# Kernel tuning notes

Hardware: AMD Instinct MI355X
Metric: run time of the kernel (lower is better)

## Reference

```python
import jax, jax.numpy as jnp
import numpy as np

C_IN, LAT, OUT, EMB = 3, 64, 512, 5
B, H = 128, 128
KS = [4, 4, 3, 4, 2]                       # per-layer dynamic kernel sizes
CHANS = [C_IN, LAT, LAT * 2, LAT * 4, LAT * 8]  # in-channels of each dyn conv
MIX = [(C_IN, LAT), (LAT, LAT * 2), (LAT * 2, LAT * 4), (LAT * 4, LAT * 8), (LAT * 8, OUT)]


def setup_inputs() -> dict:
    key = jax.random.key(0)
    ks = jax.random.split(key, 40)
    nrm = lambda k, shape, s=0.02: jax.random.normal(k, shape, jnp.float32) * s
    inp = {}
    inp["input"] = jax.random.normal(ks[0], (B, C_IN, H, H), jnp.float32)
    inp["label"] = jax.random.randint(ks[1], (B,), 0, 10)
    inp["emb"] = nrm(ks[2], (10, EMB), 1.0)  # label embedding table
    i = 3
    for j, (c, k) in enumerate(zip(CHANS, KS), 1):  # label -> dyn kernel linears
        inp[f"l{j}_w"] = nrm(ks[i], (EMB, c * k * k), 0.1)
        inp[f"l{j}_b"] = jnp.zeros((c * k * k,), jnp.float32)
        i += 1
    for j, (ci, co) in enumerate(MIX, 1):  # channel-mixer linears
        inp[f"cm{j}_w"] = nrm(ks[i], (ci, co))
        inp[f"cm{j}_b"] = jnp.zeros((co,), jnp.float32)
        i += 1
    for j, c in enumerate([LAT, LAT * 2, LAT * 4, LAT * 8], 1):  # BN affine params
        inp[f"bn{j}_g"] = jnp.ones((c,), jnp.float32)
        inp[f"bn{j}_b"] = jnp.zeros((c,), jnp.float32)
    return inp


def dw_conv(x, k, stride, pad):
    """Per-sample, per-channel (depthwise) 2d cross-correlation.
    x: (B,C,H,W), k: (B,C,h,w) -> (B,C,H',W')."""
    def one(xi, ki):
        return jax.lax.conv_general_dilated(
            xi[None], ki[:, None], (stride, stride),
            [(pad, pad), (pad, pad)],
            dimension_numbers=("NCHW", "OIHW", "NCHW"),
            feature_group_count=xi.shape[0])[0]
    return jax.vmap(one)(x, k)


def reference(input, label, emb,
              l1_w, l1_b, l2_w, l2_b, l3_w, l3_b, l4_w, l4_b, l5_w, l5_b,
              cm1_w, cm1_b, cm2_w, cm2_b, cm3_w, cm3_b, cm4_w, cm4_b, cm5_w, cm5_b,
              bn1_g, bn1_b, bn2_g, bn2_b, bn3_g, bn3_b, bn4_g, bn4_b):
    e = emb[label]  # (B, EMB)
    dk = lambda w, b, c, k: jnp.tanh(e @ w + b).reshape(-1, c, k, k)
    k1 = dk(l1_w, l1_b, C_IN, 4)
    k2 = dk(l2_w, l2_b, LAT, 4)
    k3 = dk(l3_w, l3_b, LAT * 2, 3)
    k4 = dk(l4_w, l4_b, LAT * 4, 4)
    k5 = dk(l5_w, l5_b, LAT * 8, 2)

    mix = lambda z, w, b: jnp.einsum("bchw,cd->bdhw", z, w) + b[None, :, None, None]
    lrelu = lambda z: jax.nn.leaky_relu(z, 0.2)

    def bn(z, g, b):  # training-mode BN (batch statistics, biased var, eps=1e-5)
        m = z.mean((0, 2, 3), keepdims=True)
        v = z.var((0, 2, 3), keepdims=True)
        return (z - m) * jax.lax.rsqrt(v + 1e-5) * g[None, :, None, None] + b[None, :, None, None]

    z = bn(lrelu(mix(dw_conv(input, k1, 2, 1), cm1_w, cm1_b)), bn1_g, bn1_b)
    z = bn(lrelu(mix(dw_conv(z, k2, 2, 1), cm2_w, cm2_b)), bn2_g, bn2_b)
    z = bn(lrelu(mix(dw_conv(z, k3, 2, 1), cm3_w, cm3_b)), bn3_g, bn3_b)
    z = bn(lrelu(mix(dw_conv(z, k4, 2, 1), cm4_w, cm4_b)), bn4_g, bn4_b)
    z = jax.nn.sigmoid(mix(dw_conv(z, k5, 1, 0), cm5_w, cm5_b))  # (B, OUT, 7, 7)
    return (z, label)
```

## Files before the change

### kernel.cpp

```cpp
#include <hip/hip_runtime.h>
#include <hip/hip_bf16.h>

typedef __hip_bfloat16 bf16;
using short8  = __attribute__((ext_vector_type(8))) short;
using floatx4 = __attribute__((ext_vector_type(4))) float;

__device__ __forceinline__ float b2f(unsigned short u) {
    union { unsigned int i; float f; } v; v.i = ((unsigned int)u) << 16; return v.f;
}
__device__ __forceinline__ unsigned short f2b(float f) {
    bf16 h = __float2bfloat16(f);
    return *(unsigned short*)&h;
}

#define NREP 16

__global__ __launch_bounds__(256) void prep_kernel(
    const int* __restrict__ label, const float* __restrict__ emb,
    const float* __restrict__ l1w, const float* __restrict__ l1b,
    const float* __restrict__ l2w, const float* __restrict__ l2b,
    const float* __restrict__ l3w, const float* __restrict__ l3b,
    const float* __restrict__ l4w, const float* __restrict__ l4b,
    const float* __restrict__ l5w, const float* __restrict__ l5b,
    float* __restrict__ dynk, float* __restrict__ stats,
    float* __restrict__ labelOut)
{
    const int tid = threadIdx.x;
    if (blockIdx.x == gridDim.x - 1) {
        for (int i = tid; i < 30720; i += 256) stats[i] = 0.0f;
        if (tid < 128) labelOut[tid] = (float)label[tid];
        return;
    }
    int idx = blockIdx.x * 256 + tid;
    if (idx >= 1071104) return;
    const float* w; const float* bb; int loc, ckk, ksk, base;
    if (idx < 6144)        { w = l1w; bb = l1b; loc = idx;          ckk = 48;   ksk = 0;  base = 0;      }
    else if (idx < 137216) { w = l2w; bb = l2b; loc = idx - 6144;   ckk = 1024; ksk = 16; base = 6144;   }
    else if (idx < 284672) { w = l3w; bb = l3b; loc = idx - 137216; ckk = 1152; ksk = 9;  base = 137216; }
    else if (idx < 808960) { w = l4w; bb = l4b; loc = idx - 284672; ckk = 4096; ksk = 16; base = 284672; }
    else                   { w = l5w; bb = l5b; loc = idx - 808960; ckk = 2048; ksk = 4;  base = 808960; }
    int b   = loc / ckk;
    int col = loc - b * ckk;
    int lab = label[b];
    float acc = bb[col];
    #pragma unroll
    for (int m = 0; m < 5; ++m)
        acc = fmaf(emb[lab * 5 + m], w[m * ckk + col], acc);
    float val = tanhf(acc);
    if (ksk == 0) {
        dynk[idx] = val;
    } else {
        int c  = col / ksk;
        int t  = col - c * ksk;
        int Cl = ckk / ksk;
        dynk[base + b * ckk + t * Cl + c] = val;
    }
}

__global__ void bn_prep(const float* __restrict__ st,
                        const float* __restrict__ gam, const float* __restrict__ bet,
                        float* __restrict__ aff, int C, float NINV)
{
    int c = threadIdx.x;
    if (c >= C) return;
    float s = 0.f, q = 0.f;
    #pragma unroll
    for (int r = 0; r < NREP; ++r) {
        s += st[r * 2 * C + c];
        q += st[r * 2 * C + C + c];
    }
    float m   = s * NINV;
    float var = fmaf(q, NINV, -m * m);
    float sc  = gam[c] * rsqrtf(var + 1e-5f);
    aff[c]     = sc;
    aff[C + c] = fmaf(-m, sc, bet[c]);
}

__global__ __launch_bounds__(256) void wt_kernel(
    const float* __restrict__ w2, const float* __restrict__ w3,
    const float* __restrict__ w4, const float* __restrict__ w5,
    bf16* __restrict__ wt2, bf16* __restrict__ wt3,
    bf16* __restrict__ wt4, bf16* __restrict__ wt5)
{
    __shared__ float T[32][33];
    const int tid = threadIdx.x;
    int t = blockIdx.x;
    const float* W; bf16* WT; int K, N, tl;
    if (t < 8)        { W = w2; WT = wt2; K = 64;  N = 128; tl = t; }
    else if (t < 40)  { W = w3; WT = wt3; K = 128; N = 256; tl = t - 8; }
    else if (t < 168) { W = w4; WT = wt4; K = 256; N = 512; tl = t - 40; }
    else              { W = w5; WT = wt5; K = 512; N = 512; tl = t - 168; }
    const int NT = N >> 5;
    const int kt = tl / NT, nt = tl - kt * NT;
    const int k0 = kt * 32, n0 = nt * 32;
    const int cc = tid & 31, rr = tid >> 5;
    #pragma unroll
    for (int it = 0; it < 4; ++it) {
        int k = rr + it * 8;
        T[k][cc] = W[(long)(k0 + k) * N + n0 + cc];
    }
    __syncthreads();
    #pragma unroll
    for (int it = 0; it < 4; ++it) {
        int n = rr + it * 8;
        WT[(long)(n0 + n) * K + k0 + cc] = __float2bfloat16(T[cc][n]);
    }
}

__global__ __launch_bounds__(128) void fused_l1_v3(
    const float* __restrict__ xf, const float* __restrict__ dynk,
    const float* __restrict__ W, const float* __restrict__ bias,
    bf16* __restrict__ y, float* __restrict__ statsOut)
{
    constexpr int HIN = 128, HOUT = 64;
    constexpr int TW = 16, TH = 8;
    constexpr int PS  = 36;
    constexpr int PCH = 18 * PS;

    __shared__ float patch[3 * PCH];
    __shared__ __align__(16) float dwT[16 * 28];
    __shared__ float Wlds[192];
    __shared__ float klds[48];
    __shared__ float biasL[64];
    __shared__ float sums[64], sqs[64];

    const int tid = threadIdx.x;
    const int b   = blockIdx.x >> 5;
    const int tl  = blockIdx.x & 31;
    const int ty0 = (tl >> 2) * TH;
    const int tx0 = (tl & 3) * TW;

    if (tid < 48) klds[tid] = dynk[b * 48 + tid];
    for (int i = tid; i < 192; i += 128) Wlds[i] = W[i];
    if (tid < 64) { biasL[tid] = bias[tid]; sums[tid] = 0.f; sqs[tid] = 0.f; }

    {
        const int iy0 = ty0 * 2 - 1, ix0 = tx0 * 2 - 1;
        for (int i = tid; i < 3 * 18 * 34; i += 128) {
            int c  = i / 612;
            int r  = i - c * 612;
            int py = r / 34, px = r - py * 34;
            int gy = iy0 + py, gx = ix0 + px;
            float v = 0.f;
            if ((unsigned)gy < (unsigned)HIN && (unsigned)gx < (unsigned)HIN)
                v = xf[((long)b * 3 + c) * (HIN * HIN) + gy * HIN + gx];
            patch[c * PCH + py * PS + px] = v;
        }
    }
    __syncthreads();

    {
        const int py = tid >> 4, px = tid & 15;
        const int pixg = tid >> 3, j = tid & 7;
        #pragma unroll
        for (int c = 0; c < 3; ++c) {
            const float* pb = &patch[c * PCH + (py * 2) * PS + px * 2];
            float a = 0.f;
            #pragma unroll
            for (int kh = 0; kh < 4; ++kh)
                #pragma unroll
                for (int kw = 0; kw < 4; ++kw)
                    a = fmaf(pb[kh * PS + kw], klds[c * 16 + kh * 4 + kw], a);
            dwT[pixg * 28 + j * 3 + c] = a;
        }
    }
    __syncthreads();

    {
        const int cq = tid & 7, pixg = tid >> 3;
        const int d0 = cq * 8;
        float Wr[3][8], bi[8];
        #pragma unroll
        for (int c = 0; c < 3; ++c)
            #pragma unroll
            for (int t = 0; t < 8; ++t) Wr[c][t] = Wlds[c * 64 + d0 + t];
        #pragma unroll
        for (int t = 0; t < 8; ++t) bi[t] = biasL[d0 + t];

        float dv[24];
        #pragma unroll
        for (int q4 = 0; q4 < 6; ++q4)
            *(float4*)&dv[q4 * 4] = *(const float4*)&dwT[pixg * 28 + q4 * 4];

        float sreg[8] = {}, qreg[8] = {};
        #pragma unroll
        for (int j = 0; j < 8; ++j) {
            const int pos = pixg * 8 + j;
            const float dv0 = dv[j * 3 + 0];
            const float dv1 = dv[j * 3 + 1];
            const float dv2 = dv[j * 3 + 2];
            const int py = pos >> 4, px = pos & 15;
            const long row = ((long)(b * HOUT + ty0 + py)) * HOUT + tx0 + px;
            union { uint4 v; unsigned short us[8]; } pk;
            #pragma unroll
            for (int t = 0; t < 8; ++t) {
                float v = fmaf(dv0, Wr[0][t], fmaf(dv1, Wr[1][t], fmaf(dv2, Wr[2][t], bi[t])));
                v = v > 0.f ? v : 0.2f * v;
                sreg[t] += v;
                qreg[t] = fmaf(v, v, qreg[t]);
                pk.us[t] = f2b(v);
            }
            *(uint4*)&y[row * 64 + d0] = pk.v;
        }
        #pragma unroll
        for (int m = 8; m < 64; m <<= 1)
            #pragma unroll
            for (int t = 0; t < 8; ++t) {
                sreg[t] += __shfl_xor(sreg[t], m);
                qreg[t] += __shfl_xor(qreg[t], m);
            }
        if ((tid & 63) < 8) {
            #pragma unroll
            for (int t = 0; t < 8; ++t) {
                atomicAdd(&sums[d0 + t], sreg[t]);
                atomicAdd(&sqs [d0 + t], qreg[t]);
            }
        }
    }
    __syncthreads();
    {
        const int rep = blockIdx.x & (NREP - 1);
        if (tid < 64) {
            atomicAdd(&statsOut[rep * 128 + tid],      sums[tid]);
            atomicAdd(&statsOut[rep * 128 + 64 + tid], sqs[tid]);
        }
    }
}

template<int C, int KS, int HIN, int HOUT, int STRIDE, int PAD, int NTHR>
__global__ __launch_bounds__(NTHR) void dw_direct(
    const bf16* __restrict__ x, const float* __restrict__ aff,
    const float* __restrict__ dynkT, bf16* __restrict__ outA)
{
    constexpr int G   = C / 8;
    constexpr int KSK = KS * KS;
    static_assert(NTHR == HOUT * G, "one output row per block");

    __shared__ __align__(16) float wlds[KSK * C];

    const int tid = threadIdx.x;
    const int b   = blockIdx.x / HOUT;
    const int oy  = blockIdx.x % HOUT;

    {
        const float* src = dynkT + (long)b * (KSK * C);
        for (int i = tid * 4; i < KSK * C; i += NTHR * 4)
            *(float4*)&wlds[i] = *(const float4*)&src[i];
    }
    __syncthreads();

    const int g  = tid % G;
    const int ox = tid / G;
    const int c0 = g * 8;
    const int iy0 = oy * STRIDE - PAD;
    const int ix0 = ox * STRIDE - PAD;

    float sc[8], sh[8];
    {
        float4 a0 = *(const float4*)&aff[c0];
        float4 a1 = *(const float4*)&aff[c0 + 4];
        float4 b0 = *(const float4*)&aff[C + c0];
        float4 b1 = *(const float4*)&aff[C + c0 + 4];
        sc[0]=a0.x; sc[1]=a0.y; sc[2]=a0.z; sc[3]=a0.w;
        sc[4]=a1.x; sc[5]=a1.y; sc[6]=a1.z; sc[7]=a1.w;
        sh[0]=b0.x; sh[1]=b0.y; sh[2]=b0.z; sh[3]=b0.w;
        sh[4]=b1.x; sh[5]=b1.y; sh[6]=b1.z; sh[7]=b1.w;
    }

    float acc[8];
    #pragma unroll
    for (int ch = 0; ch < 8; ++ch) acc[ch] = 0.f;

    const bool interior = (iy0 >= 0) && (iy0 + KS <= HIN) &&
                          (ix0 >= 0) && (ix0 + KS <= HIN);

    if (interior) {
        const bf16* bp = x + ((long)(b * HIN + iy0) * HIN + ix0) * C + c0;
        uint4 v[KSK];
        #pragma unroll
        for (int kh = 0; kh < KS; ++kh)
            #pragma unroll
            for (int kw = 0; kw < KS; ++kw)
                v[kh * KS + kw] = *(const uint4*)(bp + (kh * HIN + kw) * C);
        #pragma unroll
        for (int t = 0; t < KSK; ++t) {
            const float* wp = &wlds[t * C + c0];
            float4 wa = *(const float4*)wp;
            float4 wb = *(const float4*)(wp + 4);
            const float wt[8] = {wa.x, wa.y, wa.z, wa.w, wb.x, wb.y, wb.z, wb.w};
            #pragma unroll
            for (int ch = 0; ch < 8; ++ch) {
                unsigned u = ((const unsigned*)&v[t])[ch >> 1];
                unsigned bits = (ch & 1) ? (u & 0xffff0000u) : (u << 16);
                float xb = fmaf(__uint_as_float(bits), sc[ch], sh[ch]);
                acc[ch] = fmaf(xb, wt[ch], acc[ch]);
            }
        }
    } else {
        #pragma unroll
        for (int kh = 0; kh < KS; ++kh) {
            const int iy = iy0 + kh;
            if ((unsigned)iy >= (unsigned)HIN) continue;
            #pragma unroll
            for (int kw = 0; kw < KS; ++kw) {
                const int ix = ix0 + kw;
                if ((unsigned)ix >= (unsigned)HIN) continue;
                uint4 v = *(const uint4*)&x[((long)(b * HIN + iy) * HIN + ix) * C + c0];
                const float* wp = &wlds[(kh * KS + kw) * C + c0];
                float4 wa = *(const float4*)wp;
                float4 wb = *(const float4*)(wp + 4);
                const float wt[8] = {wa.x, wa.y, wa.z, wa.w, wb.x, wb.y, wb.z, wb.w};
                #pragma unroll
                for (int ch = 0; ch < 8; ++ch) {
                    unsigned u = ((const unsigned*)&v)[ch >> 1];
                    unsigned bits = (ch & 1) ? (u & 0xffff0000u) : (u << 16);
                    float xb = fmaf(__uint_as_float(bits), sc[ch], sh[ch]);
                    acc[ch] = fmaf(xb, wt[ch], acc[ch]);
                }
            }
        }
    }

    union { uint4 v; unsigned short us[8]; } pk;
    #pragma unroll
    for (int ch = 0; ch < 8; ++ch) pk.us[ch] = f2b(acc[ch]);
    *(uint4*)&outA[((long)(b * HOUT + oy) * HOUT + ox) * C + c0] = pk.v;
}

template<int K, int COUT, bool LAST>
__global__ __launch_bounds__(256) void gemm_layer(
    const bf16* __restrict__ A, const bf16* __restrict__ WT,
    const float* __restrict__ bias, bf16* __restrict__ y,
    float* __restrict__ statsOut, float* __restrict__ outF, int Mtiles)
{
    constexpr int SK = 72;
    constexpr int CS = 136;
    __shared__ __align__(16) unsigned short smem[18432];
    unsigned short* As  = smem;
    unsigned short* Bs  = smem + 9216;
    unsigned short* Csh = smem;
    __shared__ float sums[128], sqs[128];

    const int tid  = threadIdx.x;
    const int lane = tid & 63;
    const int w    = tid >> 6;
    const int wm   = (w >> 1) * 64, wn = (w & 1) * 64;
    const int lm   = lane & 15, lq = lane >> 4;
    const int mt   = blockIdx.x % Mtiles;
    const int nt   = blockIdx.x / Mtiles;
    const long m0  = (long)mt * 128;
    const int  n0  = nt * 128;

    floatx4 acc[4][4];
    #pragma unroll
    for (int i = 0; i < 4; ++i)
        #pragma unroll
        for (int j = 0; j < 4; ++j) acc[i][j] = (floatx4)0.0f;

    for (int kb = 0; kb < K; kb += 64) {
        __syncthreads();
        #pragma unroll
        for (int s = 0; s < 4; ++s) {
            int i = tid + s * 256;
            int m = i >> 3, q = i & 7;
            uint4 va = *(const uint4*)(A  + ((m0 + m) * K + kb + q * 8));
            uint4 vb = *(const uint4*)(WT + ((long)(n0 + m) * K + kb + q * 8));
            *(uint4*)&As[m * SK + q * 8] = va;
            *(uint4*)&Bs[m * SK + q * 8] = vb;
        }
        __syncthreads();
        #pragma unroll
        for (int h = 0; h < 2; ++h) {
            short8 af[4], bfr[4];
            #pragma unroll
            for (int i = 0; i < 4; ++i) {
                af[i]  = *(const short8*)&As[(wm + i * 16 + lm) * SK + h * 32 + lq * 8];
                bfr[i] = *(const short8*)&Bs[(wn + i * 16 + lm) * SK + h * 32 + lq * 8];
            }
            #pragma unroll
            for (int i = 0; i < 4; ++i)
                #pragma unroll
                for (int j = 0; j < 4; ++j)
                    acc[i][j] = __builtin_amdgcn_mfma_f32_16x16x32_bf16(af[i], bfr[j], acc[i][j], 0, 0, 0);
        }
    }
    __syncthreads();

    float bj[4];
    #pragma unroll
    for (int j = 0; j < 4; ++j) bj[j] = bias[n0 + wn + j * 16 + lm];

    if constexpr (!LAST) {
        if (tid < 128) { sums[tid] = 0.f; sqs[tid] = 0.f; }
        #pragma unroll
        for (int i = 0; i < 4; ++i)
            #pragma unroll
            for (int j = 0; j < 4; ++j) {
                int c = wn + j * 16 + lm;
                #pragma unroll
                for (int rg = 0; rg < 4; ++rg) {
                    int r = wm + i * 16 + lq * 4 + rg;
                    float v = acc[i][j][rg] + bj[j];
                    v = v > 0.f ? v : 0.2f * v;
                    Csh[r * CS + c] = f2b(v);
                }
            }
        __syncthreads();
        const int cg = tid & 15, mr = tid >> 4;
        float sacc[8], qacc[8];
        #pragma unroll
        for (int t = 0; t < 8; ++t) { sacc[t] = 0.f; qacc[t] = 0.f; }
        #pragma unroll
        for (int it = 0; it < 8; ++it) {
            int m = mr + it * 16;
            uint4 pk = *(const uint4*)&Csh[m * CS + cg * 8];
            *(uint4*)&y[(m0 + m) * COUT + n0 + cg * 8] = pk;
            const unsigned short* pu = (const unsigned short*)&pk;
            #pragma unroll
            for (int t = 0; t < 8; ++t) {
                float f = b2f(pu[t]);
                sacc[t] += f;
                qacc[t] = fmaf(f, f, qacc[t]);
            }
        }
        #pragma unroll
        for (int t = 0; t < 8; ++t) {
            atomicAdd(&sums[cg * 8 + t], sacc[t]);
            atomicAdd(&sqs [cg * 8 + t], qacc[t]);
        }
        __syncthreads();
        {
            const int rep = blockIdx.x & (NREP - 1);
            if (tid < 128) {
                atomicAdd(&statsOut[rep * 2 * COUT + n0 + tid],        sums[tid]);
                atomicAdd(&statsOut[rep * 2 * COUT + COUT + n0 + tid], sqs[tid]);
            }
        }
    } else {
        #pragma unroll
        for (int i = 0; i < 4; ++i)
            #pragma unroll
            for (int j = 0; j < 4; ++j) {
                int c  = wn + j * 16 + lm;
                int rb = wm + i * 16 + lq * 4;
                ushort4 pk;
                unsigned short* pp = (unsigned short*)&pk;
                #pragma unroll
                for (int rg = 0; rg < 4; ++rg)
                    pp[rg] = f2b(acc[i][j][rg] + bj[j]);
                *(ushort4*)&Csh[c * CS + rb] = pk;
            }
        __syncthreads();
        const int mg = tid & 15, nr = tid >> 4;
        #pragma unroll
        for (int it = 0; it < 8; ++it) {
            int n = nr + it * 16;
            uint4 pk = *(const uint4*)&Csh[n * CS + mg * 8];
            const unsigned short* pu = (const unsigned short*)&pk;
            #pragma unroll
            for (int t = 0; t < 8; ++t) {
                int m = (int)m0 + mg * 8 + t;
                int b = m / 49, pos = m - b * 49;
                float v = b2f(pu[t]);
                outF[((long)(b * 512 + n0 + n)) * 49 + pos] = 1.f / (1.f + __expf(-v));
            }
        }
    }
}


extern "C" void kernel_launch(void* const* d_in, const int* in_sizes, int n_in,
                              void* d_out, int out_size, void* d_ws, size_t ws_size,
                              hipStream_t stream)
{
    const float* input = (const float*)d_in[0];
    const int*   label = (const int*)d_in[1];
    const float* emb   = (const float*)d_in[2];
    const float* lw[5] = {(const float*)d_in[3], (const float*)d_in[5], (const float*)d_in[7],
                          (const float*)d_in[9], (const float*)d_in[11]};
    const float* lb[5] = {(const float*)d_in[4], (const float*)d_in[6], (const float*)d_in[8],
                          (const float*)d_in[10], (const float*)d_in[12]};
    const float* cmw[5] = {(const float*)d_in[13], (const float*)d_in[15], (const float*)d_in[17],
                           (const float*)d_in[19], (const float*)d_in[21]};
    const float* cmb[5] = {(const float*)d_in[14], (const float*)d_in[16], (const float*)d_in[18],
                           (const float*)d_in[20], (const float*)d_in[22]};
    const float* bng[4] = {(const float*)d_in[23], (const float*)d_in[25],
                           (const float*)d_in[27], (const float*)d_in[29]};
    const float* bnb[4] = {(const float*)d_in[24], (const float*)d_in[26],
                           (const float*)d_in[28], (const float*)d_in[30]};
    float* out = (float*)d_out;

    float* wsf   = (float*)d_ws;
    float* dynk  = wsf;
    float* stats = wsf + 1071104;
    const float* k1  = dynk;
    const float* k2T = dynk + 6144;
    const float* k3T = dynk + 137216;
    const float* k4T = dynk + 284672;
    const float* k5T = dynk + 808960;
    float* st1 = stats;
    float* st2 = stats + 2048;
    float* st3 = stats + 6144;
    float* st4 = stats + 14336;

    bf16* wt  = (bf16*)((char*)d_ws + 4407296);
    bf16* wt2 = wt;
    bf16* wt3 = wt + 8192;
    bf16* wt4 = wt + 40960;
    bf16* wt5 = wt + 172032;
    bf16* S1  = (bf16*)((char*)d_ws + 5308416);
    bf16* S2  = (bf16*)((char*)d_ws + 72417280);
    float* affBase = (float*)((char*)d_ws + 89194496);
    float* aff1 = affBase;
    float* aff2 = affBase + 128;
    float* aff3 = affBase + 384;
    float* aff4 = affBase + 896;

    prep_kernel<<<4186, 256, 0, stream>>>(label, emb,
        lw[0], lb[0], lw[1], lb[1], lw[2], lb[2], lw[3], lb[3], lw[4], lb[4],
        dynk, stats, out + 3211264);
    wt_kernel<<<424, 256, 0, stream>>>(cmw[1], cmw[2], cmw[3], cmw[4],
                                       wt2, wt3, wt4, wt5);

    fused_l1_v3<<<4096, 128, 0, stream>>>(input, k1, cmw[0], cmb[0], S1, st1);

    bn_prep<<<1, 64, 0, stream>>>(st1, bng[0], bnb[0], aff1, 64, 1.f / 524288.f);
    dw_direct<64, 4, 64, 32, 2, 1, 256><<<4096, 256, 0, stream>>>(S1, aff1, k2T, S2);
    gemm_layer<64, 128, false><<<1024, 256, 0, stream>>>(
        S2, wt2, cmb[1], S1, st2, nullptr, 1024);

    bn_prep<<<1, 128, 0, stream>>>(st2, bng[1], bnb[1], aff2, 128, 1.f / 131072.f);
    dw_direct<128, 3, 32, 16, 2, 1, 256><<<2048, 256, 0, stream>>>(S1, aff2, k3T, S2);
    gemm_layer<128, 256, false><<<512, 256, 0, stream>>>(
        S2, wt3, cmb[2], S1, st3, nullptr, 256);

    bn_prep<<<1, 256, 0, stream>>>(st3, bng[2], bnb[2], aff3, 256, 1.f / 32768.f);
    dw_direct<256, 4, 16, 8, 2, 1, 256><<<1024, 256, 0, stream>>>(S1, aff3, k4T, S2);
    gemm_layer<256, 512, false><<<256, 256, 0, stream>>>(
        S2, wt4, cmb[3], S1, st4, nullptr, 64);

    bn_prep<<<1, 512, 0, stream>>>(st4, bng[3], bnb[3], aff4, 512, 1.f / 8192.f);
    dw_direct<512, 2, 8, 7, 1, 0, 448><<<896, 448, 0, stream>>>(S1, aff4, k5T, S2);
    gemm_layer<512, 512, true><<<196, 256, 0, stream>>>(
        S2, wt5, cmb[4], nullptr, nullptr, out, 49);
}
```

Baseline: 328.3 us.

## Fold BN stat finalization into producer kernels via last-block atomic counter

Removes the four separate single-block bn_prep launches. Each producer kernel (layer-1 fused kernel and the GEMM layers) now increments a global counter after publishing its partial statistics, and the last block to finish computes the BN scale and shift. This saves launch gaps and tiny serial kernels, at the cost of an extra fence, an atomic per block and a tail of work on one block. It also unrolls the patch-load loop with predicates and writes leaky ReLU as fmaxf.

```diff
diff --git a/kernel.cpp b/kernel.cpp
--- a/kernel.cpp
+++ b/kernel.cpp
@@ -23,11 +23,12 @@
     const float* __restrict__ l4w, const float* __restrict__ l4b,
     const float* __restrict__ l5w, const float* __restrict__ l5b,
     float* __restrict__ dynk, float* __restrict__ stats,
-    float* __restrict__ labelOut)
+    unsigned* __restrict__ cnts, float* __restrict__ labelOut)
 {
     const int tid = threadIdx.x;
     if (blockIdx.x == gridDim.x - 1) {
         for (int i = tid; i < 30720; i += 256) stats[i] = 0.0f;
+        if (tid < 4) cnts[tid] = 0u;
         if (tid < 128) labelOut[tid] = (float)label[tid];
         return;
     }
@@ -55,25 +56,6 @@
         int Cl = ckk / ksk;
         dynk[base + b * ckk + t * Cl + c] = val;
     }
-}
-
-__global__ void bn_prep(const float* __restrict__ st,
-                        const float* __restrict__ gam, const float* __restrict__ bet,
-                        float* __restrict__ aff, int C, float NINV)
-{
-    int c = threadIdx.x;
-    if (c >= C) return;
-    float s = 0.f, q = 0.f;
-    #pragma unroll
-    for (int r = 0; r < NREP; ++r) {
-        s += st[r * 2 * C + c];
-        q += st[r * 2 * C + C + c];
-    }
-    float m   = s * NINV;
-    float var = fmaf(q, NINV, -m * m);
-    float sc  = gam[c] * rsqrtf(var + 1e-5f);
-    aff[c]     = sc;
-    aff[C + c] = fmaf(-m, sc, bet[c]);
 }
 
 __global__ __launch_bounds__(256) void wt_kernel(
@@ -107,10 +89,12 @@
     }
 }
 
-__global__ __launch_bounds__(128) void fused_l1_v3(
+__global__ __launch_bounds__(128) void fused_l1_v4(
     const float* __restrict__ xf, const float* __restrict__ dynk,
     const float* __restrict__ W, const float* __restrict__ bias,
-    bf16* __restrict__ y, float* __restrict__ statsOut)
+    bf16* __restrict__ y, float* __restrict__ statsOut,
+    const float* __restrict__ gam, const float* __restrict__ bet,
+    float* __restrict__ aff, unsigned* __restrict__ cnt, int nblk)
 {
     constexpr int HIN = 128, HOUT = 64;
     constexpr int TW = 16, TH = 8;
@@ -123,6 +107,7 @@
     __shared__ float klds[48];
     __shared__ float biasL[64];
     __shared__ float sums[64], sqs[64];
+    __shared__ int lastFlag;
 
     const int tid = threadIdx.x;
     const int b   = blockIdx.x >> 5;
@@ -136,15 +121,18 @@
 
     {
         const int iy0 = ty0 * 2 - 1, ix0 = tx0 * 2 - 1;
-        for (int i = tid; i < 3 * 18 * 34; i += 128) {
+        #pragma unroll
+        for (int k = 0; k < 15; ++k) {
+            int i  = tid + k * 128;
             int c  = i / 612;
             int r  = i - c * 612;
             int py = r / 34, px = r - py * 34;
             int gy = iy0 + py, gx = ix0 + px;
+            bool slot = (i < 1836);
+            bool inb  = slot && ((unsigned)gy < (unsigned)HIN) && ((unsigned)gx < (unsigned)HIN);
             float v = 0.f;
-            if ((unsigned)gy < (unsigned)HIN && (unsigned)gx < (unsigned)HIN)
-                v = xf[((long)b * 3 + c) * (HIN * HIN) + gy * HIN + gx];
-            patch[c * PCH + py * PS + px] = v;
+            if (inb) v = xf[((long)b * 3 + c) * (HIN * HIN) + gy * HIN + gx];
+            if (slot) patch[c * PCH + py * PS + px] = v;
         }
     }
     __syncthreads();
@@ -195,7 +183,7 @@
             #pragma unroll
             for (int t = 0; t < 8; ++t) {
                 float v = fmaf(dv0, Wr[0][t], fmaf(dv1, Wr[1][t], fmaf(dv2, Wr[2][t], bi[t])));
-                v = v > 0.f ? v : 0.2f * v;
+                v = fmaxf(v, 0.2f * v);
                 sreg[t] += v;
                 qreg[t] = fmaf(v, v, qreg[t]);
                 pk.us[t] = f2b(v);
@@ -224,6 +212,28 @@
             atomicAdd(&statsOut[rep * 128 + tid],      sums[tid]);
             atomicAdd(&statsOut[rep * 128 + 64 + tid], sqs[tid]);
         }
+    }
+    __syncthreads();
+    if (tid == 0) {
+        __threadfence();
+        unsigned old = atomicAdd(cnt, 1u);
+        lastFlag = (old == (unsigned)(nblk - 1)) ? 1 : 0;
+    }
+    __syncthreads();
+    if (lastFlag && tid < 64) {
+        const int c = tid;
+        float s = 0.f, q = 0.f;
+        #pragma unroll
+        for (int r = 0; r < NREP; ++r) {
+            s += atomicAdd(&statsOut[r * 128 + c], 0.0f);
+            q += atomicAdd(&statsOut[r * 128 + 64 + c], 0.0f);
+        }
+        const float NINV = 1.f / 524288.f;
+        float m   = s * NINV;
+        float var = fmaf(q, NINV, -m * m);
+        float sc  = gam[c] * rsqrtf(var + 1e-5f);
+        aff[c]      = sc;
+        aff[64 + c] = fmaf(-m, sc, bet[c]);
     }
 }
 
@@ -331,7 +341,9 @@
 __global__ __launch_bounds__(256) void gemm_layer(
     const bf16* __restrict__ A, const bf16* __restrict__ WT,
     const float* __restrict__ bias, bf16* __restrict__ y,
-    float* __restrict__ statsOut, float* __restrict__ outF, int Mtiles)
+    float* __restrict__ statsOut, float* __restrict__ outF, int Mtiles,
+    const float* __restrict__ gam, const float* __restrict__ bet,
+    float* __restrict__ aff, unsigned* __restrict__ cnt, float NINV, int nblk)
 {
     constexpr int SK = 72;
     constexpr int CS = 136;
@@ -340,6 +352,7 @@
     unsigned short* Bs  = smem + 9216;
     unsigned short* Csh = smem;
     __shared__ float sums[128], sqs[128];
+    __shared__ int lastFlag;
 
     const int tid  = threadIdx.x;
     const int lane = tid & 63;
@@ -401,7 +414,7 @@
                 for (int rg = 0; rg < 4; ++rg) {
                     int r = wm + i * 16 + lq * 4 + rg;
                     float v = acc[i][j][rg] + bj[j];
-                    v = v > 0.f ? v : 0.2f * v;
+                    v = fmaxf(v, 0.2f * v);
                     Csh[r * CS + c] = f2b(v);
                 }
             }
@@ -434,6 +447,28 @@
             if (tid < 128) {
                 atomicAdd(&statsOut[rep * 2 * COUT + n0 + tid],        sums[tid]);
                 atomicAdd(&statsOut[rep * 2 * COUT + COUT + n0 + tid], sqs[tid]);
+            }
+        }
+        __syncthreads();
+        if (tid == 0) {
+            __threadfence();
+            unsigned old = atomicAdd(cnt, 1u);
+            lastFlag = (old == (unsigned)(nblk - 1)) ? 1 : 0;
+        }
+        __syncthreads();
+        if (lastFlag) {
+            for (int c = tid; c < COUT; c += 256) {
+                float s = 0.f, q = 0.f;
+                #pragma unroll
+                for (int r = 0; r < NREP; ++r) {
+                    s += atomicAdd(&statsOut[r * 2 * COUT + c], 0.0f);
+                    q += atomicAdd(&statsOut[r * 2 * COUT + COUT + c], 0.0f);
+                }
+                float m   = s * NINV;
+                float var = fmaf(q, NINV, -m * m);
+                float sc  = gam[c] * rsqrtf(var + 1e-5f);
+                aff[c]        = sc;
+                aff[COUT + c] = fmaf(-m, sc, bet[c]);
             }
         }
     } else {
@@ -515,32 +550,34 @@
     float* aff2 = affBase + 128;
     float* aff3 = affBase + 384;
     float* aff4 = affBase + 896;
+    unsigned* cnts = (unsigned*)((char*)d_ws + 89202176);
 
     prep_kernel<<<4186, 256, 0, stream>>>(label, emb,
         lw[0], lb[0], lw[1], lb[1], lw[2], lb[2], lw[3], lb[3], lw[4], lb[4],
-        dynk, stats, out + 3211264);
+        dynk, stats, cnts, out + 3211264);
     wt_kernel<<<424, 256, 0, stream>>>(cmw[1], cmw[2], cmw[3], cmw[4],
                                        wt2, wt3, wt4, wt5);
 
-    fused_l1_v3<<<4096, 128, 0, stream>>>(input, k1, cmw[0], cmb[0], S1, st1);
-
-    bn_prep<<<1, 64, 0, stream>>>(st1, bng[0], bnb[0], aff1, 64, 1.f / 524288.f);
+    fused_l1_v4<<<4096, 128, 0, stream>>>(input, k1, cmw[0], cmb[0], S1, st1,
+                                          bng[0], bnb[0], aff1, cnts + 0, 4096);
+
     dw_direct<64, 4, 64, 32, 2, 1, 256><<<4096, 256, 0, stream>>>(S1, aff1, k2T, S2);
     gemm_layer<64, 128, false><<<1024, 256, 0, stream>>>(
-        S2, wt2, cmb[1], S1, st2, nullptr, 1024);
-
-    bn_prep<<<1, 128, 0, stream>>>(st2, bng[1], bnb[1], aff2, 128, 1.f / 131072.f);
+        S2, wt2, cmb[1], S1, st2, nullptr, 1024,
+        bng[1], bnb[1], aff2, cnts + 1, 1.f / 131072.f, 1024);
+
     dw_direct<128, 3, 32, 16, 2, 1, 256><<<2048, 256, 0, stream>>>(S1, aff2, k3T, S2);
     gemm_layer<128, 256, false><<<512, 256, 0, stream>>>(
-        S2, wt3, cmb[2], S1, st3, nullptr, 256);
-
-    bn_prep<<<1, 256, 0, stream>>>(st3, bng[2], bnb[2], aff3, 256, 1.f / 32768.f);
+        S2, wt3, cmb[2], S1, st3, nullptr, 256,
+        bng[2], bnb[2], aff3, cnts + 2, 1.f / 32768.f, 512);
+
     dw_direct<256, 4, 16, 8, 2, 1, 256><<<1024, 256, 0, stream>>>(S1, aff3, k4T, S2);
     gemm_layer<256, 512, false><<<256, 256, 0, stream>>>(
-        S2, wt4, cmb[3], S1, st4, nullptr, 64);
-
-    bn_prep<<<1, 512, 0, stream>>>(st4, bng[3], bnb[3], aff4, 512, 1.f / 8192.f);
+        S2, wt4, cmb[3], S1, st4, nullptr, 64,
+        bng[3], bnb[3], aff4, cnts + 3, 1.f / 8192.f, 256);
+
     dw_direct<512, 2, 8, 7, 1, 0, 448><<<896, 448, 0, stream>>>(S1, aff4, k5T, S2);
     gemm_layer<512, 512, true><<<196, 256, 0, stream>>>(
-        S2, wt5, cmb[4], nullptr, nullptr, out, 49);
-}
+        S2, wt5, cmb[4], nullptr, nullptr, out, 49,
+        nullptr, nullptr, nullptr, nullptr, 0.f, 0);
+}
```

Result: slower. 481.6 us (+46.7%).
